# Performance work log

Hardware: AMD Instinct MI355X
Metric: run time of the kernel (lower is better)

The kernel has to match this reference:

```python
import jax, jax.numpy as jnp
import numpy as np

N_NODES = 50000
N_EDGES = 800000
IN_C = 512
OUT_C = 256
DEC_D = 256
MASK_RATE = 0.5
NUM_MASK = int(N_NODES * MASK_RATE)


def _gcn_conv(h_in, W, b, src, dst, dinv, n):
    # PyG GCNConv: add self-loops, symmetric normalization D^-1/2 (A+I) D^-1/2
    h = h_in @ W                                   # [N, out]
    coef = (dinv[src] * dinv[dst])[:, None]        # [E, 1]
    agg = jax.ops.segment_sum(h[src] * coef, dst, num_segments=n)
    agg = agg + h * (dinv * dinv)[:, None]         # self-loop term
    return agg + b


def setup_inputs() -> dict:
    key = jax.random.key(0)
    ks = jax.random.split(key, 9)
    x = jax.random.normal(ks[0], (N_NODES, IN_C), dtype=jnp.float32)
    edge_index = jax.random.randint(ks[1], (2, N_EDGES), 0, N_NODES, dtype=jnp.int32)
    perm = jax.random.permutation(ks[2], N_NODES)
    mask_indices = perm[:NUM_MASK].astype(jnp.int32)
    mask_token = jax.random.normal(ks[3], (1, IN_C), dtype=jnp.float32)
    s_enc = 1.0 / np.sqrt(IN_C)
    enc_W = jax.random.uniform(ks[4], (IN_C, OUT_C), jnp.float32, -s_enc, s_enc)
    enc_b = jnp.zeros((OUT_C,), jnp.float32)
    s_dec = 1.0 / np.sqrt(OUT_C)
    dec_W = jax.random.uniform(ks[5], (OUT_C, DEC_D), jnp.float32, -s_dec, s_dec)
    dec_b = jnp.zeros((DEC_D,), jnp.float32)
    s_mlp = 1.0 / np.sqrt(DEC_D)
    mlp_W = jax.random.uniform(ks[6], (DEC_D, IN_C), jnp.float32, -s_mlp, s_mlp)
    mlp_b = jax.random.uniform(ks[7], (IN_C,), jnp.float32, -s_mlp, s_mlp)
    return {"x": x, "edge_index": edge_index, "mask_indices": mask_indices,
            "mask_token": mask_token, "enc_W": enc_W, "enc_b": enc_b,
            "dec_W": dec_W, "dec_b": dec_b, "mlp_W": mlp_W, "mlp_b": mlp_b}


def reference(x, edge_index, mask_indices, mask_token, enc_W, enc_b, dec_W, dec_b, mlp_W, mlp_b):
    src, dst = edge_index[0], edge_index[1]
    n = x.shape[0]
    # degree with self-loops (shared by both GCN layers)
    deg = jax.ops.segment_sum(jnp.ones((N_EDGES,), x.dtype), dst, num_segments=n) + 1.0
    dinv = jax.lax.rsqrt(deg)
    # mask nodes: replace masked rows with learned mask token
    x_masked = x.at[mask_indices].set(mask_token[0])
    # encoder: GCNConv(in_c -> out_c)
    z = _gcn_conv(x_masked, enc_W, enc_b, src, dst, dinv, n)
    # decoder: GCNConv(out_c -> dec_d) -> relu -> linear(dec_d -> in_c)
    h = jax.nn.relu(_gcn_conv(z, dec_W, dec_b, src, dst, dinv, n))
    x_recon = h @ mlp_W + mlp_b
    return (x_recon, x, mask_indices)
```

## Files before the change

kernel.cpp:

```cpp
#include <hip/hip_runtime.h>
#include <math.h>

#define NNODES 50000
#define NEDGES 800000
#define INC 512
#define OUTC 256
#define DECD 256
#define NMASK 25000

#define SCAN_B 1024
#define NSCAN ((NNODES + SCAN_B - 1) / SCAN_B)

typedef __attribute__((ext_vector_type(8))) short short8;
typedef __attribute__((ext_vector_type(4))) float f32x4;

__device__ __forceinline__ unsigned short f2bf(float f) {
    unsigned int u = __float_as_uint(f);
    u = (u + 0x7fff + ((u >> 16) & 1)) >> 16;
    return (unsigned short)u;
}
__device__ __forceinline__ float bf2f(unsigned short u) {
    return __uint_as_float(((unsigned int)u) << 16);
}


__global__ void count_deg_k(const int* __restrict__ dst, int* __restrict__ deg) {
    int e = blockIdx.x * blockDim.x + threadIdx.x;
    if (e < NEDGES) atomicAdd(&deg[dst[e]], 1);
}

__global__ __launch_bounds__(1024) void scan_part_k(const int* __restrict__ deg,
                                                    int* __restrict__ bsum,
                                                    float* __restrict__ dinv) {
    int i = blockIdx.x * SCAN_B + threadIdx.x;
    int v = (i < NNODES) ? deg[i] : 0;
    if (i < NNODES) dinv[i] = rsqrtf((float)v + 1.0f);
    int lane = threadIdx.x & 63, w = threadIdx.x >> 6;
    int s = v;
#pragma unroll
    for (int d = 32; d > 0; d >>= 1) s += __shfl_down(s, d, 64);
    __shared__ int ws[16];
    if (lane == 0) ws[w] = s;
    __syncthreads();
    if (threadIdx.x == 0) {
        int tot = 0;
#pragma unroll
        for (int j = 0; j < 16; ++j) tot += ws[j];
        bsum[blockIdx.x] = tot;
    }
}

__global__ __launch_bounds__(64) void scan_carry_k(const int* __restrict__ bsum,
                                                   int* __restrict__ bcarry,
                                                   int* __restrict__ offs) {
    int t = threadIdx.x;
    int v = (t < NSCAN) ? bsum[t] : 0;
    int incl = v;
#pragma unroll
    for (int d = 1; d < 64; d <<= 1) {
        int u = __shfl_up(incl, d, 64);
        if (t >= d) incl += u;
    }
    if (t < NSCAN) bcarry[t] = incl - v;
    if (t == 63) offs[NNODES] = incl;
}

__global__ __launch_bounds__(1024) void scan_fin_k(const int* __restrict__ deg,
                                                   const int* __restrict__ bcarry,
                                                   int* __restrict__ offs,
                                                   int* __restrict__ cursor) {
    int i = blockIdx.x * SCAN_B + threadIdx.x;
    int v = (i < NNODES) ? deg[i] : 0;
    int lane = threadIdx.x & 63, w = threadIdx.x >> 6;
    int incl = v;
#pragma unroll
    for (int d = 1; d < 64; d <<= 1) {
        int u = __shfl_up(incl, d, 64);
        if (lane >= d) incl += u;
    }
    __shared__ int ws[16];
    if (lane == 63) ws[w] = incl;
    __syncthreads();
    int carry = bcarry[blockIdx.x];
    for (int j = 0; j < w; ++j) carry += ws[j];
    int ex = carry + incl - v;
    if (i < NNODES) { offs[i] = ex; cursor[i] = ex; }
}

__global__ void fill_csr_k(const int* __restrict__ src, const int* __restrict__ dst,
                           const float* __restrict__ dinv, int* __restrict__ cursor,
                           int2* __restrict__ edges) {
    int e = blockIdx.x * blockDim.x + threadIdx.x;
    if (e >= NEDGES) return;
    int s = src[e], d = dst[e];
    int pos = atomicAdd(&cursor[d], 1);
    edges[pos] = make_int2(s, __float_as_int(dinv[s] * dinv[d]));
}


__global__ void cvt_copy_k(const float4* __restrict__ in, float4* __restrict__ outx,
                           ushort4* __restrict__ outbf, int n4) {
    int i = blockIdx.x * blockDim.x + threadIdx.x;
    if (i >= n4) return;
    float4 v = in[i];
    outx[i] = v;
    ushort4 u;
    u.x = f2bf(v.x); u.y = f2bf(v.y); u.z = f2bf(v.z); u.w = f2bf(v.w);
    outbf[i] = u;
}

__global__ void wt_k(const float* __restrict__ W, unsigned short* __restrict__ Wt,
                     int K, int N) {
    int o = blockIdx.x * blockDim.x + threadIdx.x;
    if (o >= K * N) return;
    int n = o / K;
    int k = o - n * K;
    Wt[o] = f2bf(W[(size_t)k * N + n]);
}

__global__ void token_k(const float* __restrict__ token, const float* __restrict__ W,
                        float* __restrict__ outv) {
    int j = threadIdx.x;
    float s = 0.f;
    for (int k = 0; k < INC; ++k) s += token[k] * W[(size_t)k * OUTC + j];
    outv[j] = s;
}

__global__ __launch_bounds__(64) void maskfix_bf_k(const int* __restrict__ idx,
                                                   const float* __restrict__ tokh,
                                                   unsigned short* __restrict__ h1) {
    int r = idx[blockIdx.x];
    int t = threadIdx.x;
    float4 v = *(const float4*)(tokh + t * 4);
    ushort4 u;
    u.x = f2bf(v.x); u.y = f2bf(v.y); u.z = f2bf(v.z); u.w = f2bf(v.w);
    *(ushort4*)(h1 + (size_t)r * OUTC + t * 4) = u;
}

__global__ void maskout_k(const int* __restrict__ idx, float* __restrict__ out) {
    int i = blockIdx.x * blockDim.x + threadIdx.x;
    if (i < NMASK) out[i] = (float)idx[i];
}


__global__ __launch_bounds__(256) void gemm_bf16_k(const unsigned short* __restrict__ A,
                                                   const unsigned short* __restrict__ Bt,
                                                   void* __restrict__ Cout,
                                                   int M, int K, int N,
                                                   const float* __restrict__ bias,
                                                   int out_bf16) {
    __shared__ unsigned short As[128 * 32];
    __shared__ unsigned short Bs[128 * 32];
    const int t = threadIdx.x;
    const int lane = t & 63, wv = t >> 6;
    const int bm = blockIdx.y * 128;
    const int bn = blockIdx.x * 128;
    const int wm = (wv >> 1) * 64, wn = (wv & 1) * 64;
    const int lr = lane & 15, lq = lane >> 4;

    f32x4 acc[4][4] = {};

    for (int k0 = 0; k0 < K; k0 += 32) {
        __syncthreads();
#pragma unroll
        for (int r = 0; r < 2; ++r) {
            int idx = r * 256 + wv * 64 + lane;
            int row = idx >> 2;
            int c8 = (idx & 3) * 8;
            int ga = bm + row;
            if (ga >= M) ga = M - 1;
            const unsigned short* gA = A + (size_t)ga * K + k0 + c8;
            const unsigned short* gB = Bt + (size_t)(bn + row) * K + k0 + c8;
            __builtin_amdgcn_global_load_lds(
                (const __attribute__((address_space(1))) unsigned int*)gA,
                (__attribute__((address_space(3))) unsigned int*)&As[(r * 256 + wv * 64) * 8],
                16, 0, 0);
            __builtin_amdgcn_global_load_lds(
                (const __attribute__((address_space(1))) unsigned int*)gB,
                (__attribute__((address_space(3))) unsigned int*)&Bs[(r * 256 + wv * 64) * 8],
                16, 0, 0);
        }
        __syncthreads();

        short8 av[4], bv[4];
#pragma unroll
        for (int mt = 0; mt < 4; ++mt)
            av[mt] = *(const short8*)&As[(wm + mt * 16 + lr) * 32 + lq * 8];
#pragma unroll
        for (int nt = 0; nt < 4; ++nt)
            bv[nt] = *(const short8*)&Bs[(wn + nt * 16 + lr) * 32 + lq * 8];
#pragma unroll
        for (int mt = 0; mt < 4; ++mt)
#pragma unroll
            for (int nt = 0; nt < 4; ++nt)
                acc[mt][nt] = __builtin_amdgcn_mfma_f32_16x16x32_bf16(
                    av[mt], bv[nt], acc[mt][nt], 0, 0, 0);
    }

    float* Cf = (float*)Cout;
    unsigned short* Cb = (unsigned short*)Cout;
#pragma unroll
    for (int nt = 0; nt < 4; ++nt) {
        int col = bn + wn + nt * 16 + lr;
        float bv_ = bias ? bias[col] : 0.f;
#pragma unroll
        for (int mt = 0; mt < 4; ++mt) {
            int row0 = bm + wm + mt * 16 + lq * 4;
#pragma unroll
            for (int reg = 0; reg < 4; ++reg) {
                int row = row0 + reg;
                if (row >= M) continue;
                float v = acc[mt][nt][reg] + bv_;
                if (out_bf16) Cb[(size_t)row * N + col] = f2bf(v);
                else          Cf[(size_t)row * N + col] = v;
            }
        }
    }
}


__global__ __launch_bounds__(64) void agg_bf_k(const unsigned short* __restrict__ h,
                                               unsigned short* __restrict__ out,
                                               const float* __restrict__ bias,
                                               const float* __restrict__ dinv,
                                               const int* __restrict__ offs,
                                               const int2* __restrict__ edges,
                                               int do_relu) {
    int node = blockIdx.x;
    int t = threadIdx.x;
    int beg = offs[node], end = offs[node + 1];
    float a0 = 0.f, a1 = 0.f, a2 = 0.f, a3 = 0.f;
    for (int e = beg; e < end; ++e) {
        int2 ev = edges[e];
        int s = ev.x;
        float c = __int_as_float(ev.y);
        ushort4 v = *(const ushort4*)(h + (size_t)s * OUTC + t * 4);
        a0 += bf2f(v.x) * c; a1 += bf2f(v.y) * c;
        a2 += bf2f(v.z) * c; a3 += bf2f(v.w) * c;
    }
    float di = dinv[node];
    float sc = di * di;
    ushort4 hv = *(const ushort4*)(h + (size_t)node * OUTC + t * 4);
    float4 bv = *(const float4*)(bias + t * 4);
    a0 += bf2f(hv.x) * sc + bv.x;
    a1 += bf2f(hv.y) * sc + bv.y;
    a2 += bf2f(hv.z) * sc + bv.z;
    a3 += bf2f(hv.w) * sc + bv.w;
    if (do_relu) {
        a0 = fmaxf(a0, 0.f); a1 = fmaxf(a1, 0.f);
        a2 = fmaxf(a2, 0.f); a3 = fmaxf(a3, 0.f);
    }
    ushort4 u;
    u.x = f2bf(a0); u.y = f2bf(a1); u.z = f2bf(a2); u.w = f2bf(a3);
    *(ushort4*)(out + (size_t)node * OUTC + t * 4) = u;
}


extern "C" void kernel_launch(void* const* d_in, const int* in_sizes, int n_in,
                              void* d_out, int out_size, void* d_ws, size_t ws_size,
                              hipStream_t stream) {
    const float* x    = (const float*)d_in[0];
    const int*   eidx = (const int*)d_in[1];
    const int*   midx = (const int*)d_in[2];
    const float* mtok = (const float*)d_in[3];
    const float* encW = (const float*)d_in[4];
    const float* encB = (const float*)d_in[5];
    const float* decW = (const float*)d_in[6];
    const float* decB = (const float*)d_in[7];
    const float* mlpW = (const float*)d_in[8];
    const float* mlpB = (const float*)d_in[9];
    const int* srcs = eidx;
    const int* dsts = eidx + NEDGES;

    char* ws = (char*)d_ws;
    unsigned short* x_bf  = (unsigned short*)(ws + 0);
    unsigned short* hA_bf = (unsigned short*)(ws + 51200000);
    unsigned short* hB_bf = (unsigned short*)(ws + 76800000);
    int*   deg    = (int*)  (ws + 102400000);
    float* dinv   = (float*)(ws + 102600000);
    int*   offs   = (int*)  (ws + 102800000);
    int*   cursor = (int*)  (ws + 103000064);
    int2*  edges  = (int2*) (ws + 103200064);
    float* tokh   = (float*)(ws + 109600064);
    unsigned short* encWt = (unsigned short*)(ws + 109601088);
    unsigned short* decWt = (unsigned short*)(ws + 109863232);
    unsigned short* mlpWt = (unsigned short*)(ws + 109994304);
    int*   bsum   = (int*)  (ws + 110256448);
    int*   bcarry = (int*)  (ws + 110256704);

    float* out_recon = (float*)d_out;
    float* out_x     = out_recon + (size_t)NNODES * INC;
    float* out_mask  = out_x + (size_t)NNODES * INC;

    hipMemsetAsync(deg, 0, NNODES * sizeof(int), stream);
    count_deg_k<<<(NEDGES + 255) / 256, 256, 0, stream>>>(dsts, deg);
    scan_part_k<<<NSCAN, SCAN_B, 0, stream>>>(deg, bsum, dinv);
    scan_carry_k<<<1, 64, 0, stream>>>(bsum, bcarry, offs);
    scan_fin_k<<<NSCAN, SCAN_B, 0, stream>>>(deg, bcarry, offs, cursor);
    fill_csr_k<<<(NEDGES + 255) / 256, 256, 0, stream>>>(srcs, dsts, dinv, cursor, edges);

    token_k<<<1, 256, 0, stream>>>(mtok, encW, tokh);

    cvt_copy_k<<<(NNODES * INC / 4 + 255) / 256, 256, 0, stream>>>(
        (const float4*)x, (float4*)out_x, (ushort4*)x_bf, NNODES * INC / 4);
    wt_k<<<(INC * OUTC + 255) / 256, 256, 0, stream>>>(encW, encWt, INC, OUTC);
    wt_k<<<(OUTC * DECD + 255) / 256, 256, 0, stream>>>(decW, decWt, OUTC, DECD);
    wt_k<<<(DECD * INC + 255) / 256, 256, 0, stream>>>(mlpW, mlpWt, DECD, INC);

    gemm_bf16_k<<<dim3(OUTC / 128, (NNODES + 127) / 128), 256, 0, stream>>>(
        x_bf, encWt, hA_bf, NNODES, INC, OUTC, nullptr, 1);
    maskfix_bf_k<<<NMASK, 64, 0, stream>>>(midx, tokh, hA_bf);

    agg_bf_k<<<NNODES, 64, 0, stream>>>(hA_bf, hB_bf, encB, dinv, offs, edges, 0);

    gemm_bf16_k<<<dim3(DECD / 128, (NNODES + 127) / 128), 256, 0, stream>>>(
        hB_bf, decWt, hA_bf, NNODES, OUTC, DECD, nullptr, 1);

    agg_bf_k<<<NNODES, 64, 0, stream>>>(hA_bf, hB_bf, decB, dinv, offs, edges, 1);

    gemm_bf16_k<<<dim3(INC / 128, (NNODES + 127) / 128), 256, 0, stream>>>(
        hB_bf, mlpWt, out_recon, NNODES, DECD, INC, mlpB, 0);

    maskout_k<<<(NMASK + 255) / 256, 256, 0, stream>>>(midx, out_mask);
}
```

Before: 694.5 us.

## Merge small kernels, parallelize token GEMV, pack aggregation blocks and unroll edges

```diff
diff --git a/kernel.cpp b/kernel.cpp
--- a/kernel.cpp
+++ b/kernel.cpp
@@ -89,9 +89,11 @@
 
 __global__ void fill_csr_k(const int* __restrict__ src, const int* __restrict__ dst,
                            const float* __restrict__ dinv, int* __restrict__ cursor,
-                           int2* __restrict__ edges) {
+                           int2* __restrict__ edges,
+                           const int* __restrict__ midx, float* __restrict__ out_mask) {
     int e = blockIdx.x * blockDim.x + threadIdx.x;
     if (e >= NEDGES) return;
+    if (e < NMASK) out_mask[e] = (float)midx[e];
     int s = src[e], d = dst[e];
     int pos = atomicAdd(&cursor[d], 1);
     edges[pos] = make_int2(s, __float_as_int(dinv[s] * dinv[d]));
@@ -109,21 +111,39 @@
     outbf[i] = u;
 }
 
-__global__ void wt_k(const float* __restrict__ W, unsigned short* __restrict__ Wt,
-                     int K, int N) {
+__global__ void wt3_k(const float* __restrict__ encW, const float* __restrict__ decW,
+                      const float* __restrict__ mlpW,
+                      unsigned short* __restrict__ encWt, unsigned short* __restrict__ decWt,
+                      unsigned short* __restrict__ mlpWt) {
     int o = blockIdx.x * blockDim.x + threadIdx.x;
-    if (o >= K * N) return;
-    int n = o / K;
-    int k = o - n * K;
-    Wt[o] = f2bf(W[(size_t)k * N + n]);
-}
-
-__global__ void token_k(const float* __restrict__ token, const float* __restrict__ W,
-                        float* __restrict__ outv) {
-    int j = threadIdx.x;
+    if (o < 131072) {
+        int n = o >> 9, k = o & 511;
+        encWt[o] = f2bf(encW[(size_t)k * OUTC + n]);
+    } else if (o < 131072 + 65536) {
+        int o2 = o - 131072;
+        int n = o2 >> 8, k = o2 & 255;
+        decWt[o2] = f2bf(decW[(size_t)k * DECD + n]);
+    } else if (o < 131072 + 65536 + 131072) {
+        int o2 = o - 131072 - 65536;
+        int n = o2 >> 8, k = o2 & 255;
+        mlpWt[o2] = f2bf(mlpW[(size_t)k * INC + n]);
+    }
+}
+
+__global__ __launch_bounds__(64) void token_k(const float* __restrict__ token,
+                                              const float* __restrict__ W,
+                                              float* __restrict__ outv) {
+    int j = blockIdx.x;
+    int l = threadIdx.x;
     float s = 0.f;
-    for (int k = 0; k < INC; ++k) s += token[k] * W[(size_t)k * OUTC + j];
-    outv[j] = s;
+#pragma unroll
+    for (int i = 0; i < INC / 64; ++i) {
+        int k = i * 64 + l;
+        s += token[k] * W[(size_t)k * OUTC + j];
+    }
+#pragma unroll
+    for (int d = 32; d > 0; d >>= 1) s += __shfl_down(s, d, 64);
+    if (l == 0) outv[j] = s;
 }
 
 __global__ __launch_bounds__(64) void maskfix_bf_k(const int* __restrict__ idx,
@@ -135,11 +155,6 @@
     ushort4 u;
     u.x = f2bf(v.x); u.y = f2bf(v.y); u.z = f2bf(v.z); u.w = f2bf(v.w);
     *(ushort4*)(h1 + (size_t)r * OUTC + t * 4) = u;
-}
-
-__global__ void maskout_k(const int* __restrict__ idx, float* __restrict__ out) {
-    int i = blockIdx.x * blockDim.x + threadIdx.x;
-    if (i < NMASK) out[i] = (float)idx[i];
 }
 
 
@@ -219,25 +234,40 @@
 }
 
 
-__global__ __launch_bounds__(64) void agg_bf_k(const unsigned short* __restrict__ h,
-                                               unsigned short* __restrict__ out,
-                                               const float* __restrict__ bias,
-                                               const float* __restrict__ dinv,
-                                               const int* __restrict__ offs,
-                                               const int2* __restrict__ edges,
-                                               int do_relu) {
-    int node = blockIdx.x;
-    int t = threadIdx.x;
+__global__ __launch_bounds__(256) void agg_bf_k(const unsigned short* __restrict__ h,
+                                                unsigned short* __restrict__ out,
+                                                const float* __restrict__ bias,
+                                                const float* __restrict__ dinv,
+                                                const int* __restrict__ offs,
+                                                const int2* __restrict__ edges,
+                                                int do_relu) {
+    int node = blockIdx.x * 4 + (threadIdx.x >> 6);
+    if (node >= NNODES) return;
+    int t = threadIdx.x & 63;
     int beg = offs[node], end = offs[node + 1];
     float a0 = 0.f, a1 = 0.f, a2 = 0.f, a3 = 0.f;
-    for (int e = beg; e < end; ++e) {
+    float b0 = 0.f, b1 = 0.f, b2 = 0.f, b3 = 0.f;
+    int e = beg;
+    for (; e + 2 <= end; e += 2) {
+        int2 ev0 = edges[e];
+        int2 ev1 = edges[e + 1];
+        ushort4 v0 = *(const ushort4*)(h + (size_t)ev0.x * OUTC + t * 4);
+        ushort4 v1 = *(const ushort4*)(h + (size_t)ev1.x * OUTC + t * 4);
+        float c0 = __int_as_float(ev0.y);
+        float c1 = __int_as_float(ev1.y);
+        a0 += bf2f(v0.x) * c0; a1 += bf2f(v0.y) * c0;
+        a2 += bf2f(v0.z) * c0; a3 += bf2f(v0.w) * c0;
+        b0 += bf2f(v1.x) * c1; b1 += bf2f(v1.y) * c1;
+        b2 += bf2f(v1.z) * c1; b3 += bf2f(v1.w) * c1;
+    }
+    if (e < end) {
         int2 ev = edges[e];
-        int s = ev.x;
+        ushort4 v = *(const ushort4*)(h + (size_t)ev.x * OUTC + t * 4);
         float c = __int_as_float(ev.y);
-        ushort4 v = *(const ushort4*)(h + (size_t)s * OUTC + t * 4);
         a0 += bf2f(v.x) * c; a1 += bf2f(v.y) * c;
         a2 += bf2f(v.z) * c; a3 += bf2f(v.w) * c;
     }
+    a0 += b0; a1 += b1; a2 += b2; a3 += b3;
     float di = dinv[node];
     float sc = di * di;
     ushort4 hv = *(const ushort4*)(h + (size_t)node * OUTC + t * 4);
@@ -297,29 +327,27 @@
     scan_part_k<<<NSCAN, SCAN_B, 0, stream>>>(deg, bsum, dinv);
     scan_carry_k<<<1, 64, 0, stream>>>(bsum, bcarry, offs);
     scan_fin_k<<<NSCAN, SCAN_B, 0, stream>>>(deg, bcarry, offs, cursor);
-    fill_csr_k<<<(NEDGES + 255) / 256, 256, 0, stream>>>(srcs, dsts, dinv, cursor, edges);
-
-    token_k<<<1, 256, 0, stream>>>(mtok, encW, tokh);
+    fill_csr_k<<<(NEDGES + 255) / 256, 256, 0, stream>>>(srcs, dsts, dinv, cursor, edges,
+                                                         midx, out_mask);
+
+    token_k<<<256, 64, 0, stream>>>(mtok, encW, tokh);
 
     cvt_copy_k<<<(NNODES * INC / 4 + 255) / 256, 256, 0, stream>>>(
         (const float4*)x, (float4*)out_x, (ushort4*)x_bf, NNODES * INC / 4);
-    wt_k<<<(INC * OUTC + 255) / 256, 256, 0, stream>>>(encW, encWt, INC, OUTC);
-    wt_k<<<(OUTC * DECD + 255) / 256, 256, 0, stream>>>(decW, decWt, OUTC, DECD);
-    wt_k<<<(DECD * INC + 255) / 256, 256, 0, stream>>>(mlpW, mlpWt, DECD, INC);
+    wt3_k<<<(131072 + 65536 + 131072 + 255) / 256, 256, 0, stream>>>(
+        encW, decW, mlpW, encWt, decWt, mlpWt);
 
     gemm_bf16_k<<<dim3(OUTC / 128, (NNODES + 127) / 128), 256, 0, stream>>>(
         x_bf, encWt, hA_bf, NNODES, INC, OUTC, nullptr, 1);
     maskfix_bf_k<<<NMASK, 64, 0, stream>>>(midx, tokh, hA_bf);
 
-    agg_bf_k<<<NNODES, 64, 0, stream>>>(hA_bf, hB_bf, encB, dinv, offs, edges, 0);
+    agg_bf_k<<<(NNODES + 3) / 4, 256, 0, stream>>>(hA_bf, hB_bf, encB, dinv, offs, edges, 0);
 
     gemm_bf16_k<<<dim3(DECD / 128, (NNODES + 127) / 128), 256, 0, stream>>>(
         hB_bf, decWt, hA_bf, NNODES, OUTC, DECD, nullptr, 1);
 
-    agg_bf_k<<<NNODES, 64, 0, stream>>>(hA_bf, hB_bf, decB, dinv, offs, edges, 1);
+    agg_bf_k<<<(NNODES + 3) / 4, 256, 0, stream>>>(hA_bf, hB_bf, decB, dinv, offs, edges, 1);
 
     gemm_bf16_k<<<dim3(INC / 128, (NNODES + 127) / 128), 256, 0, stream>>>(
         hB_bf, mlpWt, out_recon, NNODES, DECD, INC, mlpB, 0);
-
-    maskout_k<<<(NMASK + 255) / 256, 256, 0, stream>>>(midx, out_mask);
-}
+}
```

Result: faster. 673.0 us (-3.1%).
